# Performance work log

Hardware: AMD Instinct MI355X
Metric: run time of the kernel (lower is better)

## Reference

```python
import jax, jax.numpy as jnp
import numpy as np

B, E, H, T = 16384, 1024, 16, 256  # batch, embed_dim, num_heads, tabular_dim
HD = E // H  # head_dim


def _mha_seq1(q, kv, Wqkv, bqkv, Wo, bo):
    """nn.MultiheadAttention with query/key/value of seq_len 1 (batch_first).
    q, kv: [B, E]; Wqkv: [3E, E]; bqkv: [3E]; Wo: [E, E]; bo: [E]."""
    Wq, Wk, Wv = jnp.split(Wqkv, 3, axis=0)
    bq, bk, bv = jnp.split(bqkv, 3)
    qp = (q @ Wq.T + bq).reshape(-1, H, HD)   # [B, H, HD]
    kp = (kv @ Wk.T + bk).reshape(-1, H, HD)
    vp = (kv @ Wv.T + bv).reshape(-1, H, HD)
    scores = jnp.sum(qp * kp, axis=-1, keepdims=True) * (1.0 / HD ** 0.5)  # [B, H, 1]
    w = jax.nn.softmax(scores, axis=-1)       # softmax over 1 key -> all ones
    out = (w * vp).reshape(-1, E)             # [B, E]
    return out @ Wo.T + bo


def setup_inputs() -> dict:
    key = jax.random.key(0)
    ks = jax.random.split(key, 16)
    s_e = 1.0 / E ** 0.5
    s_t = 1.0 / T ** 0.5
    return {
        "text_features": jax.random.normal(ks[0], (B, E), jnp.float32),
        "ecg_features": jax.random.normal(ks[1], (B, E), jnp.float32),
        "tabular_features": jax.random.normal(ks[2], (B, T), jnp.float32),
        "Wc_text": jax.random.uniform(ks[3], (E, T), jnp.float32, -s_t, s_t),
        "bc_text": jax.random.uniform(ks[4], (E,), jnp.float32, -s_t, s_t),
        "Wc_ecg": jax.random.uniform(ks[5], (E, T), jnp.float32, -s_t, s_t),
        "bc_ecg": jax.random.uniform(ks[6], (E,), jnp.float32, -s_t, s_t),
        "Wqkv_a": jax.random.uniform(ks[7], (3 * E, E), jnp.float32, -s_e, s_e),
        "bqkv_a": jnp.zeros((3 * E,), jnp.float32),
        "Wo_a": jax.random.uniform(ks[8], (E, E), jnp.float32, -s_e, s_e),
        "bo_a": jnp.zeros((E,), jnp.float32),
        "Wqkv_b": jax.random.uniform(ks[9], (3 * E, E), jnp.float32, -s_e, s_e),
        "bqkv_b": jnp.zeros((3 * E,), jnp.float32),
        "Wo_b": jax.random.uniform(ks[10], (E, E), jnp.float32, -s_e, s_e),
        "bo_b": jnp.zeros((E,), jnp.float32),
    }


def reference(text_features, ecg_features, tabular_features,
              Wc_text, bc_text, Wc_ecg, bc_ecg,
              Wqkv_a, bqkv_a, Wo_a, bo_a,
              Wqkv_b, bqkv_b, Wo_b, bo_b):
    text_scale = jax.nn.sigmoid(tabular_features @ Wc_text.T + bc_text)
    ecg_scale = jax.nn.sigmoid(tabular_features @ Wc_ecg.T + bc_ecg)
    text_query = text_features * text_scale
    ecg_query = ecg_features * ecg_scale
    attn_a = _mha_seq1(text_query, ecg_features, Wqkv_a, bqkv_a, Wo_a, bo_a)
    attn_b = _mha_seq1(ecg_query, text_features, Wqkv_b, bqkv_b, Wo_b, bo_b)
    return jnp.concatenate([attn_a, attn_b], axis=-1)
```

## Files before the change

### kernel.cpp

```cpp
#include <hip/hip_runtime.h>
#include <hip/hip_bf16.h>
#include <stdint.h>

typedef __bf16 bf16_t;
typedef bf16_t bf16x8 __attribute__((ext_vector_type(8)));
typedef bf16_t bf16x4 __attribute__((ext_vector_type(4)));
typedef float  f32x4  __attribute__((ext_vector_type(4)));

#define E_DIM 1024
#define B_ROWS 16384
#define CVT_TOTAL (2 * B_ROWS * E_DIM / 8)
#define CVT_SPLIT (1024 * 256 * 5)

__device__ __forceinline__ void gload_lds16(const void* g, void* l) {
    __builtin_amdgcn_global_load_lds(
        (const __attribute__((address_space(1))) void*)g,
        (__attribute__((address_space(3))) void*)l,
        16, 0, 0);
}

__device__ __forceinline__ void cvt_chunk(const float* __restrict__ ecg,
                                          const float* __restrict__ text,
                                          bf16_t* __restrict__ Xb, int idx) {
    const int half = CVT_TOTAL / 2;
    const float* src = (idx < half) ? ecg : text;
    int j = (idx < half) ? idx : idx - half;
    f32x4 lo = ((const f32x4*)src)[2 * j];
    f32x4 hi = ((const f32x4*)src)[2 * j + 1];
    bf16x8 v;
    v[0] = (bf16_t)lo[0]; v[1] = (bf16_t)lo[1]; v[2] = (bf16_t)lo[2]; v[3] = (bf16_t)lo[3];
    v[4] = (bf16_t)hi[0]; v[5] = (bf16_t)hi[1]; v[6] = (bf16_t)hi[2]; v[7] = (bf16_t)hi[3];
    ((bf16x8*)Xb)[idx] = v;
}

__global__ __launch_bounds__(256) void prep1_k(const float* __restrict__ ecg,
                                               const float* __restrict__ text,
                                               const float* __restrict__ Wqkv_a,
                                               const float* __restrict__ bqkv_a,
                                               const float* __restrict__ Wo_a,
                                               const float* __restrict__ bo_a,
                                               const float* __restrict__ Wqkv_b,
                                               const float* __restrict__ bqkv_b,
                                               const float* __restrict__ Wo_b,
                                               const float* __restrict__ bo_b,
                                               bf16_t* __restrict__ WoB,
                                               bf16_t* __restrict__ WvT,
                                               float* __restrict__ beff,
                                               bf16_t* __restrict__ Xb) {
    const size_t MAT = (size_t)E_DIM * E_DIM;
    __shared__ float t[64][65];
    int b = blockIdx.x;
    int tid = threadIdx.x;
    if (b < 2048) {
        const int n4 = (int)(MAT / 4);
        int i = b * 256 + tid;
        const float* src = (i < n4) ? Wo_a : Wo_b;
        int j = (i < n4) ? i : i - n4;
        f32x4 v = ((const f32x4*)src)[j];
        bf16x4 o;
        o[0] = (bf16_t)v[0]; o[1] = (bf16_t)v[1];
        o[2] = (bf16_t)v[2]; o[3] = (bf16_t)v[3];
        ((bf16x4*)WoB)[i] = o;
    } else if (b < 2560) {
        int x = b - 2048;
        int ms = x >> 8;
        const float* in = (ms ? Wqkv_b : Wqkv_a) + 2 * MAT;
        bf16_t* o = WvT + (size_t)ms * MAT;
        int bb = x & 255;
        int bx = bb & 15, by = bb >> 4;
        int j0 = by * 64, k0 = bx * 64;
#pragma unroll
        for (int p = 0; p < 4; ++p) {
            int u = tid + 256 * p;
            int r = u >> 4, c4 = u & 15;
            f32x4 v = *(const f32x4*)(in + (size_t)(j0 + r) * E_DIM + k0 + c4 * 4);
            t[r][c4 * 4 + 0] = v[0]; t[r][c4 * 4 + 1] = v[1];
            t[r][c4 * 4 + 2] = v[2]; t[r][c4 * 4 + 3] = v[3];
        }
        __syncthreads();
#pragma unroll
        for (int p = 0; p < 4; ++p) {
            int u = tid + 256 * p;
            int r = u >> 4, c4 = u & 15;
            bf16x4 ov;
            ov[0] = (bf16_t)t[c4 * 4 + 0][r];
            ov[1] = (bf16_t)t[c4 * 4 + 1][r];
            ov[2] = (bf16_t)t[c4 * 4 + 2][r];
            ov[3] = (bf16_t)t[c4 * 4 + 3][r];
            *(bf16x4*)(o + (size_t)(k0 + r) * E_DIM + j0 + c4 * 4) = ov;
        }
    } else if (b < 3072) {
        int idx = (b - 2560) * 4 + (tid >> 6);
        int lane = tid & 63;
        int sel = idx >> 10;
        int i = idx & 1023;
        const float* Wo = sel ? Wo_b : Wo_a;
        const float* bv = (sel ? bqkv_b : bqkv_a) + 2 * E_DIM;
        const float* bo = sel ? bo_b : bo_a;
        float s = 0.f;
        for (int j = lane; j < E_DIM; j += 64)
            s += Wo[(size_t)i * E_DIM + j] * bv[j];
#pragma unroll
        for (int o = 32; o > 0; o >>= 1) s += __shfl_down(s, o);
        if (lane == 0) beff[sel * E_DIM + i] = s + bo[i];
    } else {
        const int stride = 1024 * 256;
        for (int i = (b - 3072) * 256 + tid; i < CVT_SPLIT; i += stride)
            cvt_chunk(ecg, text, Xb, i);
    }
}

__global__ __launch_bounds__(256, 2) void combo_k(const float* __restrict__ ecg,
                                                  const float* __restrict__ text,
                                                  bf16_t* __restrict__ Xb,
                                                  const bf16_t* __restrict__ WoB,
                                                  const bf16_t* __restrict__ WvT,
                                                  bf16_t* __restrict__ Weff) {
    const size_t MAT = (size_t)E_DIM * E_DIM;
    __shared__ __align__(16) bf16_t As[128][64];
    __shared__ __align__(16) bf16_t Bs[128][64];

    int b = blockIdx.x;
    int tid = threadIdx.x;

    if (b >= 128) {
        const int stride = 2048 * 256;
        for (int i = CVT_SPLIT + (b - 128) * 256 + tid; i < CVT_TOTAL; i += stride)
            cvt_chunk(ecg, text, Xb, i);
        return;
    }

    int bid = b;
    int ms = bid >> 6;
    int t  = bid & 63;
    int mt = t >> 3, nt = t & 7;
    const bf16_t* A  = WoB + (size_t)ms * MAT;
    const bf16_t* Bm = WvT + (size_t)ms * MAT;
    bf16_t*       C  = Weff + (size_t)ms * MAT;
    int m0 = mt * 128, n0 = nt * 128;

    int lane = tid & 63;
    int wid = tid >> 6;
    int wrow = (wid >> 1) * 64;
    int wcol = (wid & 1) * 64;
    int cl = lane & 15;
    int rg = lane >> 4;

    f32x4 acc[4][4] = {};

    for (int kt = 0; kt < 16; ++kt) {
#pragma unroll
        for (int i = 0; i < 4; ++i) {
            int chunk = i * 256 + wid * 64 + lane;
            int row = chunk >> 3;
            int kk8 = (chunk & 7) * 8;
            char* la = (char*)(&As[0][0]) + (size_t)(i * 256 + wid * 64) * 16;
            char* lb = (char*)(&Bs[0][0]) + (size_t)(i * 256 + wid * 64) * 16;
            gload_lds16(A  + (size_t)(m0 + row) * E_DIM + kt * 64 + kk8, la);
            gload_lds16(Bm + (size_t)(n0 + row) * E_DIM + kt * 64 + kk8, lb);
        }
        __syncthreads();
#pragma unroll
        for (int ks = 0; ks < 2; ++ks) {
            int kk = ks * 32 + rg * 8;
            bf16x8 af[4], bq[4];
#pragma unroll
            for (int m = 0; m < 4; ++m) af[m] = *(const bf16x8*)(&As[wrow + m * 16 + cl][kk]);
#pragma unroll
            for (int n = 0; n < 4; ++n) bq[n] = *(const bf16x8*)(&Bs[wcol + n * 16 + cl][kk]);
#pragma unroll
            for (int m = 0; m < 4; ++m)
#pragma unroll
                for (int n = 0; n < 4; ++n)
                    acc[m][n] = __builtin_amdgcn_mfma_f32_16x16x32_bf16(af[m], bq[n], acc[m][n], 0, 0, 0);
        }
        __syncthreads();
    }

#pragma unroll
    for (int m = 0; m < 4; ++m) {
        int r = m0 + wrow + m * 16 + rg * 4;
#pragma unroll
        for (int n = 0; n < 4; ++n) {
            int c = n0 + wcol + n * 16 + cl;
#pragma unroll
            for (int j = 0; j < 4; ++j)
                C[(size_t)(r + j) * E_DIM + c] = (bf16_t)acc[m][n][j];
        }
    }
}

#define VMW(n) asm volatile("s_waitcnt vmcnt(" #n ")" ::: "memory")
#define BAR()  __builtin_amdgcn_s_barrier()

__global__ __launch_bounds__(512, 2) void main_gemm_v2_k(const bf16_t* __restrict__ Xb,
                                                         const bf16_t* __restrict__ Weff,
                                                         const float* __restrict__ beff,
                                                         float* __restrict__ out) {
    const size_t MAT  = (size_t)E_DIM * E_DIM;
    const size_t XMAT = (size_t)B_ROWS * E_DIM;

    int bid = blockIdx.x;
    int wg = (bid & 7) * 64 + (bid >> 3);
    int nt = wg & 7;
    int mt = wg >> 3;
    int sel = nt >> 2;
    int n0 = (nt & 3) * 256;
    int m0 = mt * 256;

    const bf16_t* gA = Xb + (size_t)sel * XMAT + (size_t)m0 * E_DIM;
    const bf16_t* gB = Weff + (size_t)sel * MAT + (size_t)n0 * E_DIM;
    const float*  bb = beff + sel * E_DIM;

    __shared__ __align__(16) bf16_t sA[2][256 * 64];
    __shared__ __align__(16) bf16_t sB[2][256 * 64];

    int tid  = threadIdx.x;
    int lane = tid & 63;
    int wid  = tid >> 6;
    int wr = wid >> 1;
    int wc = wid & 1;
    int cl = lane & 15;
    int rg = lane >> 4;

    int c0 = tid, c1 = 512 + tid;
    int r0 = c0 >> 3, r1 = c1 >> 3;
    int go0 = r0 * E_DIM + (((c0 & 7) * 8) ^ ((r0 & 7) << 3));
    int go1 = r1 * E_DIM + (((c1 & 7) * 8) ^ ((r1 & 7) << 3));
    int ld0 = c0 * 8, ld1 = c1 * 8;

    int koff0 = (rg * 8) ^ ((cl & 7) << 3);
    int koff1 = (32 + rg * 8) ^ ((cl & 7) << 3);

    f32x4 acc[4][8] = {};
    bf16x8 af[4], bq[4];

#define STAGE_A(kt, h, prt) do { \
    gload_lds16(gA + (size_t)((h) * 128) * E_DIM + (kt) * 64 + go0, &sA[prt][(h) * 8192 + ld0]); \
    gload_lds16(gA + (size_t)((h) * 128) * E_DIM + (kt) * 64 + go1, &sA[prt][(h) * 8192 + ld1]); } while (0)
#define STAGE_B(kt, h, prt) do { \
    gload_lds16(gB + (size_t)((h) * 128) * E_DIM + (kt) * 64 + go0, &sB[prt][(h) * 8192 + ld0]); \
    gload_lds16(gB + (size_t)((h) * 128) * E_DIM + (kt) * 64 + go1, &sB[prt][(h) * 8192 + ld1]); } while (0)
#define RD_A(p, KOFF) do { _Pragma("unroll") for (int m = 0; m < 4; ++m) \
    af[m] = *(const bf16x8*)(&sA[p][(wr * 64 + m * 16 + cl) * 64 + (KOFF)]); } while (0)
#define RD_B(p, nh, KOFF) do { _Pragma("unroll") for (int n = 0; n < 4; ++n) \
    bq[n] = *(const bf16x8*)(&sB[p][((nh) * 128 + wc * 64 + n * 16 + cl) * 64 + (KOFF)]); } while (0)
#define MM(nh) do { __builtin_amdgcn_s_setprio(1); \
    _Pragma("unroll") for (int m = 0; m < 4; ++m) _Pragma("unroll") for (int n = 0; n < 4; ++n) \
        acc[m][(nh) * 4 + n] = __builtin_amdgcn_mfma_f32_16x16x32_bf16(af[m], bq[n], acc[m][(nh) * 4 + n], 0, 0, 0); \
    __builtin_amdgcn_s_setprio(0); } while (0)

    STAGE_A(0, 0, 0); STAGE_A(0, 1, 0); STAGE_B(0, 0, 0); STAGE_B(0, 1, 0);
    VMW(2);
    BAR();

#pragma unroll
    for (int t = 0; t < 16; ++t) {
        const int p = t & 1, pn = p ^ 1;
        RD_A(p, koff0); RD_B(p, 0, koff0);
        if (t < 15) { STAGE_A(t + 1, 0, pn); VMW(2); } else { VMW(0); }
        BAR();
        MM(0);
        BAR();
        RD_B(p, 1, koff0);
        if (t < 15) STAGE_A(t + 1, 1, pn);
        BAR();
        MM(1);
        BAR();
        RD_A(p, koff1); RD_B(p, 1, koff1);
        if (t < 15) STAGE_B(t + 1, 0, pn);
        BAR();
        MM(1);
        BAR();
        RD_B(p, 0, koff1);
        if (t < 15) { STAGE_B(t + 1, 1, pn); VMW(2); }
        BAR();
        MM(0);
        BAR();
    }

#pragma unroll
    for (int m = 0; m < 4; ++m) {
        int r = m0 + wr * 64 + m * 16 + rg * 4;
#pragma unroll
        for (int ni = 0; ni < 8; ++ni) {
            int ch = n0 + (ni >> 2) * 128 + wc * 64 + (ni & 3) * 16 + cl;
            float bias = bb[ch];
            size_t gc = (size_t)sel * E_DIM + ch;
#pragma unroll
            for (int j = 0; j < 4; ++j)
                out[(size_t)(r + j) * (2 * E_DIM) + gc] = acc[m][ni][j] + bias;
        }
    }
#undef STAGE_A
#undef STAGE_B
#undef RD_A
#undef RD_B
#undef MM
}

extern "C" void kernel_launch(void* const* d_in, const int* in_sizes, int n_in,
                              void* d_out, int out_size, void* d_ws, size_t ws_size,
                              hipStream_t stream) {
    const float* text   = (const float*)d_in[0];
    const float* ecg    = (const float*)d_in[1];
    const float* Wqkv_a = (const float*)d_in[7];
    const float* bqkv_a = (const float*)d_in[8];
    const float* Wo_a   = (const float*)d_in[9];
    const float* bo_a   = (const float*)d_in[10];
    const float* Wqkv_b = (const float*)d_in[11];
    const float* bqkv_b = (const float*)d_in[12];
    const float* Wo_b   = (const float*)d_in[13];
    const float* bo_b   = (const float*)d_in[14];

    const size_t MAT  = (size_t)E_DIM * E_DIM;
    const size_t XMAT = (size_t)B_ROWS * E_DIM;
    bf16_t* WoB  = (bf16_t*)d_ws;
    bf16_t* WvT  = WoB + 2 * MAT;
    bf16_t* Weff = WvT + 2 * MAT;
    float*  beff = (float*)(Weff + 2 * MAT);
    bf16_t* Xb   = (bf16_t*)(beff + 2 * E_DIM);

    prep1_k<<<4096, 256, 0, stream>>>(ecg, text,
                                      Wqkv_a, bqkv_a, Wo_a, bo_a,
                                      Wqkv_b, bqkv_b, Wo_b, bo_b,
                                      WoB, WvT, beff, Xb);
    combo_k<<<2176, 256, 0, stream>>>(ecg, text, Xb, WoB, WvT, Weff);
    main_gemm_v2_k<<<512, 512, 0, stream>>>(Xb, Weff, beff, (float*)d_out);
}
```

Measured before the change: 134.6 us.

## Triple-buffer A tiles in main GEMM to prefetch two K-steps ahead

The main GEMM gets a third LDS buffer for the A operand so A tiles are loaded two K-iterations ahead, while B stays double-buffered one step ahead. The load issue order inside each iteration is reshuffled and the vmcnt waits are adjusted to match. The aim is to hide more global-load latency for the activation stream. In exchange it raises LDS usage, which can limit occupancy, and it relies on fragile wait-count bookkeeping.

After: 134.4 us. About the same (-0.1%).

```diff
diff --git a/kernel.cpp b/kernel.cpp
--- a/kernel.cpp
+++ b/kernel.cpp
@@ -130,9 +130,8 @@
         return;
     }
 
-    int bid = b;
-    int ms = bid >> 6;
-    int t  = bid & 63;
+    int ms = b >> 6;
+    int t  = b & 63;
     int mt = t >> 3, nt = t & 7;
     const bf16_t* A  = WoB + (size_t)ms * MAT;
     const bf16_t* Bm = WvT + (size_t)ms * MAT;
@@ -193,7 +192,7 @@
 #define VMW(n) asm volatile("s_waitcnt vmcnt(" #n ")" ::: "memory")
 #define BAR()  __builtin_amdgcn_s_barrier()
 
-__global__ __launch_bounds__(512, 2) void main_gemm_v2_k(const bf16_t* __restrict__ Xb,
+__global__ __launch_bounds__(512, 2) void main_gemm_v8_k(const bf16_t* __restrict__ Xb,
                                                          const bf16_t* __restrict__ Weff,
                                                          const float* __restrict__ beff,
                                                          float* __restrict__ out) {
@@ -212,7 +211,7 @@
     const bf16_t* gB = Weff + (size_t)sel * MAT + (size_t)n0 * E_DIM;
     const float*  bb = beff + sel * E_DIM;
 
-    __shared__ __align__(16) bf16_t sA[2][256 * 64];
+    __shared__ __align__(16) bf16_t sA[3][256 * 64];
     __shared__ __align__(16) bf16_t sB[2][256 * 64];
 
     int tid  = threadIdx.x;
@@ -250,30 +249,34 @@
         acc[m][(nh) * 4 + n] = __builtin_amdgcn_mfma_f32_16x16x32_bf16(af[m], bq[n], acc[m][(nh) * 4 + n], 0, 0, 0); \
     __builtin_amdgcn_s_setprio(0); } while (0)
 
-    STAGE_A(0, 0, 0); STAGE_A(0, 1, 0); STAGE_B(0, 0, 0); STAGE_B(0, 1, 0);
-    VMW(2);
+    STAGE_A(0, 0, 0); STAGE_A(0, 1, 0);
+    STAGE_B(0, 0, 0); STAGE_B(0, 1, 0);
+    STAGE_A(1, 0, 1); STAGE_A(1, 1, 1);
+    VMW(4);
     BAR();
 
 #pragma unroll
     for (int t = 0; t < 16; ++t) {
-        const int p = t & 1, pn = p ^ 1;
-        RD_A(p, koff0); RD_B(p, 0, koff0);
-        if (t < 15) { STAGE_A(t + 1, 0, pn); VMW(2); } else { VMW(0); }
+        const int pA = t % 3;
+        const int pB = t & 1;
+        RD_A(pA, koff0); RD_B(pB, 0, koff0);
+        if (t < 15) STAGE_B(t + 1, 0, pB ^ 1);
         BAR();
         MM(0);
         BAR();
-        RD_B(p, 1, koff0);
-        if (t < 15) STAGE_A(t + 1, 1, pn);
+        RD_B(pB, 1, koff0);
+        if (t < 15) STAGE_B(t + 1, 1, pB ^ 1);
         BAR();
         MM(1);
         BAR();
-        RD_A(p, koff1); RD_B(p, 1, koff1);
-        if (t < 15) STAGE_B(t + 1, 0, pn);
+        RD_A(pA, koff1); RD_B(pB, 1, koff1);
+        if (t < 14) STAGE_A(t + 2, 0, (t + 2) % 3);
         BAR();
         MM(1);
         BAR();
-        RD_B(p, 0, koff1);
-        if (t < 15) { STAGE_B(t + 1, 1, pn); VMW(2); }
+        RD_B(pB, 0, koff1);
+        if (t < 14)      { STAGE_A(t + 2, 1, (t + 2) % 3); VMW(4); }
+        else if (t == 14) VMW(0);
         BAR();
         MM(0);
         BAR();
@@ -326,5 +329,5 @@
                                       Wqkv_b, bqkv_b, Wo_b, bo_b,
                                       WoB, WvT, beff, Xb);
     combo_k<<<2176, 256, 0, stream>>>(ecg, text, Xb, WoB, WvT, Weff);
-    main_gemm_v2_k<<<512, 512, 0, stream>>>(Xb, Weff, beff, (float*)d_out);
-}
+    main_gemm_v8_k<<<512, 512, 0, stream>>>(Xb, Weff, beff, (float*)d_out);
+}
```
